# Kernel tuning notes

Hardware: AMD Instinct MI355X
Metric: run time of the kernel (lower is better)

Reference implementation:

```python
import jax, jax.numpy as jnp
import numpy as np

E, K, H, I = 32, 4, 2048, 1024   # experts, top_k, hidden, moe_intermediate
T = 4096                          # tokens (batch*seq flattened)
ROUTED_SCALING_FACTOR = 1.0


def setup_inputs() -> dict:
    key = jax.random.key(0)
    ks = jax.random.split(key, 5)
    return {
        "hidden_states": jax.random.normal(ks[0], (T, H), jnp.float32),
        "gate_w": jax.random.normal(ks[1], (E, H), jnp.float32) * 0.02,
        "expert_bias": jax.random.normal(ks[2], (E,), jnp.float32) * 0.01,
        "w13": jax.random.normal(ks[3], (E, 2 * I, H), jnp.float32) * 0.02,  # fused gate|up proj
        "w2": jax.random.normal(ks[4], (E, H, I), jnp.float32) * 0.02,       # down proj
    }


def reference(hidden_states, gate_w, expert_bias, w13, w2):
    x = hidden_states                                  # [T, H]
    router_logits = x @ gate_w.T                       # [T, E]
    scores = jax.nn.sigmoid(router_logits)             # sigmoid scoring
    # expert bias affects SELECTION only, not the combine weights
    _, topk_idx = jax.lax.top_k(scores + expert_bias[None, :], K)   # [T, K]
    topk_w = jnp.take_along_axis(scores, topk_idx, axis=1)          # [T, K] (bias-free weights)
    topk_w = topk_w / jnp.sum(topk_w, axis=1, keepdims=True)        # renormalize (norm_topk_prob)
    # dense combine matrix [T, E]: zero for unselected experts
    tok = jnp.arange(x.shape[0])[:, None]
    combine = jnp.zeros((x.shape[0], E), x.dtype).at[tok, topk_idx].set(topk_w)

    def expert_body(acc, ew):
        w13_e, w2_e, cw = ew                           # [2I,H], [H,I], [T]
        gu = x @ w13_e.T                               # [T, 2I]
        h = jax.nn.silu(gu[:, :I]) * gu[:, I:]         # SwiGLU
        return acc + cw[:, None] * (h @ w2_e.T), None  # weighted combine

    out, _ = jax.lax.scan(expert_body, jnp.zeros_like(x), (w13, w2, combine.T))
    return out * ROUTED_SCALING_FACTOR
```

## Files before the change

kernel.cpp:

```cpp
#include <hip/hip_runtime.h>

#define NE 32
#define NK 4
#define HD 2048
#define ID 1024
#define NT 4096
#define TKR (NT*NK)
#define BM 128
#define BK 64
#define LDA 72
#define MAXTILES 160

typedef __attribute__((ext_vector_type(8))) short short8;
typedef __attribute__((ext_vector_type(4))) float floatx4;

__device__ __forceinline__ unsigned short f2bf(float f) {
  unsigned u = __builtin_bit_cast(unsigned, f);
  unsigned r = u + 0x7fffu + ((u >> 16) & 1u);
  return (unsigned short)(r >> 16);
}

__global__ __launch_bounds__(256) void cvt_kernel(const float* __restrict__ x,
                                                  unsigned short* __restrict__ xb) {
  size_t i = ((size_t)blockIdx.x * 256 + threadIdx.x) * 8;
  if (i >= (size_t)NT * HD) return;
  float4 a = *(const float4*)(x + i);
  float4 b = *(const float4*)(x + i + 4);
  union { unsigned short s[8]; int4 v; } p;
  p.s[0]=f2bf(a.x); p.s[1]=f2bf(a.y); p.s[2]=f2bf(a.z); p.s[3]=f2bf(a.w);
  p.s[4]=f2bf(b.x); p.s[5]=f2bf(b.y); p.s[6]=f2bf(b.z); p.s[7]=f2bf(b.w);
  *(int4*)(xb + i) = p.v;
}

__global__ __launch_bounds__(256) void router_kernel(
    const float* __restrict__ x, const float* __restrict__ gate_w,
    const float* __restrict__ bias, int* __restrict__ topk_idx,
    float* __restrict__ topk_w, int* __restrict__ counts) {
  int t = blockIdx.x;
  int tid = threadIdx.x;
  int e = tid >> 3, l8 = tid & 7;
  const float* xr = x + (size_t)t * HD;
  const float* gr = gate_w + (size_t)e * HD;
  float s = 0.f;
  int base = l8 * 256;
#pragma unroll 8
  for (int i = 0; i < 256; i += 4) {
    float4 xv = *(const float4*)(xr + base + i);
    float4 gv = *(const float4*)(gr + base + i);
    s += xv.x*gv.x + xv.y*gv.y + xv.z*gv.z + xv.w*gv.w;
  }
  s += __shfl_down(s, 4, 64);
  s += __shfl_down(s, 2, 64);
  s += __shfl_down(s, 1, 64);
  __shared__ float sc[NE];
  if (l8 == 0) sc[e] = s;
  __syncthreads();
  if (tid == 0) {
    float sig[NE], sel[NE];
    for (int i = 0; i < NE; i++) {
      sig[i] = 1.f / (1.f + expf(-sc[i]));
      sel[i] = sig[i] + bias[i];
    }
    int idxs[NK]; float wsum = 0.f;
    for (int k = 0; k < NK; k++) {
      int bi = 0; float bv = -1e30f;
      for (int i = 0; i < NE; i++)
        if (sel[i] > bv) { bv = sel[i]; bi = i; }
      sel[bi] = -1e30f;
      idxs[k] = bi; wsum += sig[bi];
    }
    for (int k = 0; k < NK; k++) {
      topk_idx[t*NK + k] = idxs[k];
      topk_w[t*NK + k] = sig[idxs[k]] / wsum;
      atomicAdd(&counts[idxs[k]], 1);
    }
  }
}

__global__ void plan_kernel(const int* __restrict__ counts, int* __restrict__ offsets,
                            int* __restrict__ cursor, int* __restrict__ tiles,
                            int* __restrict__ numtiles) {
  if (threadIdx.x == 0) {
    int off = 0;
    for (int e = 0; e < NE; e++) { offsets[e] = off; off += counts[e]; cursor[e] = 0; }
    offsets[NE] = off;
    int nt = 0;
    for (int e = 0; e < NE; e++) {
      int start = offsets[e], n = counts[e];
      for (int r = 0; r < n; r += BM) {
        tiles[nt*3+0] = e; tiles[nt*3+1] = start + r; tiles[nt*3+2] = min(BM, n - r);
        nt++;
      }
    }
    *numtiles = nt;
  }
}

__global__ __launch_bounds__(256) void scatter_kernel(
    const int* __restrict__ topk_idx, const float* __restrict__ topk_w,
    const int* __restrict__ offsets, int* __restrict__ cursor,
    int* __restrict__ sorted_token, float* __restrict__ sorted_w) {
  int i = blockIdx.x * 256 + threadIdx.x;
  int e = topk_idx[i];
  int pos = offsets[e] + atomicAdd(&cursor[e], 1);
  sorted_token[pos] = i >> 2;
  sorted_w[pos] = topk_w[i];
}

__global__ __launch_bounds__(256) void gemm1_kernel(
    const unsigned short* __restrict__ xb, const float* __restrict__ w13,
    const int* __restrict__ tiles, const int* __restrict__ numtiles,
    const int* __restrict__ sorted_token, const float* __restrict__ sorted_w,
    unsigned short* __restrict__ hbuf) {
  int mt = blockIdx.y;
  if (mt >= *numtiles) return;
  int e = tiles[mt*3+0], g0 = tiles[mt*3+1], mrows = tiles[mt*3+2];
  int nb = blockIdx.x * 64;

  __shared__ unsigned short As[BM*LDA];
  __shared__ unsigned short Bs[BM*LDA];

  int tid = threadIdx.x;
  int wave = tid >> 6, lane = tid & 63;
  int m15 = lane & 15, q = lane >> 4;
  const float* w13e = w13 + (size_t)e * (2*ID) * HD;

  const unsigned short* aptr[4]; const float* bptr[4]; int sto[4];
#pragma unroll
  for (int i = 0; i < 4; i++) {
    int c = tid + 256*i;
    int r = c >> 3;
    int col = (c & 7) * 8;
    int rr = r < mrows ? r : 0;
    aptr[i] = xb + (size_t)sorted_token[g0+rr] * HD + col;
    int sr = (r < 64) ? (nb + r) : (ID + nb + r - 64);
    bptr[i] = w13e + (size_t)sr * HD + col;
    sto[i] = r * LDA + col;
  }

  floatx4 acc[2][8];
  floatx4 zf = {0.f,0.f,0.f,0.f};
#pragma unroll
  for (int mi=0;mi<2;mi++)
#pragma unroll
    for (int ni=0;ni<8;ni++) acc[mi][ni] = zf;

  for (int k0 = 0; k0 < HD; k0 += BK) {
    int4 av[4]; float4 b0[4], b1[4];
#pragma unroll
    for (int i = 0; i < 4; i++) {
      av[i] = *(const int4*)(aptr[i] + k0);
      b0[i] = *(const float4*)(bptr[i] + k0);
      b1[i] = *(const float4*)(bptr[i] + k0 + 4);
    }
#pragma unroll
    for (int i = 0; i < 4; i++) {
      *(int4*)(&As[sto[i]]) = av[i];
      union { unsigned short s[8]; int4 v; } p;
      p.s[0]=f2bf(b0[i].x); p.s[1]=f2bf(b0[i].y); p.s[2]=f2bf(b0[i].z); p.s[3]=f2bf(b0[i].w);
      p.s[4]=f2bf(b1[i].x); p.s[5]=f2bf(b1[i].y); p.s[6]=f2bf(b1[i].z); p.s[7]=f2bf(b1[i].w);
      *(int4*)(&Bs[sto[i]]) = p.v;
    }
    __syncthreads();
#pragma unroll
    for (int ks = 0; ks < 2; ks++) {
      int ko = ks*32 + q*8;
      short8 af[2], bfr[8];
#pragma unroll
      for (int mi = 0; mi < 2; mi++)
        af[mi] = *(const short8*)(&As[(wave*32 + 16*mi + m15)*LDA + ko]);
#pragma unroll
      for (int ni = 0; ni < 8; ni++)
        bfr[ni] = *(const short8*)(&Bs[(16*ni + m15)*LDA + ko]);
#pragma unroll
      for (int mi = 0; mi < 2; mi++)
#pragma unroll
        for (int ni = 0; ni < 8; ni++)
          acc[mi][ni] = __builtin_amdgcn_mfma_f32_16x16x32_bf16(af[mi], bfr[ni], acc[mi][ni], 0, 0, 0);
    }
    __syncthreads();
  }
#pragma unroll
  for (int mi = 0; mi < 2; mi++)
#pragma unroll
    for (int r = 0; r < 4; r++) {
      int row = wave*32 + 16*mi + q*4 + r;
      if (row < mrows) {
        int g = g0 + row;
        float wr = sorted_w[g];
        unsigned short* hr = hbuf + (size_t)g * ID + nb;
#pragma unroll
        for (int ni = 0; ni < 4; ni++) {
          float gv = acc[mi][ni][r];
          float uv = acc[mi][ni+4][r];
          float sg = gv / (1.f + __expf(-gv));
          hr[16*ni + m15] = f2bf(sg * uv * wr);
        }
      }
    }
}

__global__ __launch_bounds__(256) void gemm2_kernel(
    const unsigned short* __restrict__ hbuf, const float* __restrict__ w2,
    const int* __restrict__ tiles, const int* __restrict__ numtiles,
    const int* __restrict__ sorted_token, float* __restrict__ out) {
  int mt = blockIdx.y;
  if (mt >= *numtiles) return;
  int e = tiles[mt*3+0], g0 = tiles[mt*3+1], mrows = tiles[mt*3+2];
  int nb = blockIdx.x * BM;

  __shared__ unsigned short As[BM*LDA];
  __shared__ unsigned short Bs[BM*LDA];

  int tid = threadIdx.x;
  int wave = tid >> 6, lane = tid & 63;
  int m15 = lane & 15, q = lane >> 4;
  const float* w2e = w2 + (size_t)e * HD * ID;

  const unsigned short* aptr[4]; const float* bptr[4]; int sto[4];
#pragma unroll
  for (int i = 0; i < 4; i++) {
    int c = tid + 256*i;
    int r = c >> 3;
    int col = (c & 7) * 8;
    int rr = r < mrows ? r : 0;
    aptr[i] = hbuf + (size_t)(g0 + rr) * ID + col;
    bptr[i] = w2e + (size_t)(nb + r) * ID + col;
    sto[i] = r * LDA + col;
  }

  floatx4 acc[2][8];
  floatx4 zf = {0.f,0.f,0.f,0.f};
#pragma unroll
  for (int mi=0;mi<2;mi++)
#pragma unroll
    for (int ni=0;ni<8;ni++) acc[mi][ni] = zf;

  for (int k0 = 0; k0 < ID; k0 += BK) {
    int4 av[4]; float4 b0[4], b1[4];
#pragma unroll
    for (int i = 0; i < 4; i++) {
      av[i] = *(const int4*)(aptr[i] + k0);
      b0[i] = *(const float4*)(bptr[i] + k0);
      b1[i] = *(const float4*)(bptr[i] + k0 + 4);
    }
#pragma unroll
    for (int i = 0; i < 4; i++) {
      *(int4*)(&As[sto[i]]) = av[i];
      union { unsigned short s[8]; int4 v; } p;
      p.s[0]=f2bf(b0[i].x); p.s[1]=f2bf(b0[i].y); p.s[2]=f2bf(b0[i].z); p.s[3]=f2bf(b0[i].w);
      p.s[4]=f2bf(b1[i].x); p.s[5]=f2bf(b1[i].y); p.s[6]=f2bf(b1[i].z); p.s[7]=f2bf(b1[i].w);
      *(int4*)(&Bs[sto[i]]) = p.v;
    }
    __syncthreads();
#pragma unroll
    for (int ks = 0; ks < 2; ks++) {
      int ko = ks*32 + q*8;
      short8 af[2], bfr[8];
#pragma unroll
      for (int mi = 0; mi < 2; mi++)
        af[mi] = *(const short8*)(&As[(wave*32 + 16*mi + m15)*LDA + ko]);
#pragma unroll
      for (int ni = 0; ni < 8; ni++)
        bfr[ni] = *(const short8*)(&Bs[(16*ni + m15)*LDA + ko]);
#pragma unroll
      for (int mi = 0; mi < 2; mi++)
#pragma unroll
        for (int ni = 0; ni < 8; ni++)
          acc[mi][ni] = __builtin_amdgcn_mfma_f32_16x16x32_bf16(af[mi], bfr[ni], acc[mi][ni], 0, 0, 0);
    }
    __syncthreads();
  }
#pragma unroll
  for (int mi = 0; mi < 2; mi++)
#pragma unroll
    for (int r = 0; r < 4; r++) {
      int row = wave*32 + 16*mi + q*4 + r;
      if (row < mrows) {
        int tok = sorted_token[g0 + row];
        float* orow = out + (size_t)tok * HD + nb;
#pragma unroll
        for (int ni = 0; ni < 8; ni++)
          atomicAdd(&orow[16*ni + m15], acc[mi][ni][r]);
      }
    }
}

#define WS_COUNTS   0u
#define WS_CURSOR   128u
#define WS_OFFSETS  256u
#define WS_NUMTILES 512u
#define WS_TILES    1024u
#define WS_TOPKI    4096u
#define WS_TOPKW    (WS_TOPKI + TKR*4u)
#define WS_SORTTOK  (WS_TOPKW + TKR*4u)
#define WS_SORTW    (WS_SORTTOK + TKR*4u)
#define WS_XB       (WS_SORTW + TKR*4u)
#define WS_HBUF     (WS_XB + (size_t)NT*HD*2u)

extern "C" void kernel_launch(void* const* d_in, const int* in_sizes, int n_in,
                              void* d_out, int out_size, void* d_ws, size_t ws_size,
                              hipStream_t stream) {
  const float* x      = (const float*)d_in[0];
  const float* gate_w = (const float*)d_in[1];
  const float* bias   = (const float*)d_in[2];
  const float* w13    = (const float*)d_in[3];
  const float* w2     = (const float*)d_in[4];
  float* out = (float*)d_out;

  char* ws = (char*)d_ws;
  int*   counts   = (int*)(ws + WS_COUNTS);
  int*   cursor   = (int*)(ws + WS_CURSOR);
  int*   offsets  = (int*)(ws + WS_OFFSETS);
  int*   numtiles = (int*)(ws + WS_NUMTILES);
  int*   tiles    = (int*)(ws + WS_TILES);
  int*   topk_idx = (int*)(ws + WS_TOPKI);
  float* topk_w   = (float*)(ws + WS_TOPKW);
  int*   sorted_token = (int*)(ws + WS_SORTTOK);
  float* sorted_w     = (float*)(ws + WS_SORTW);
  unsigned short* xb   = (unsigned short*)(ws + WS_XB);
  unsigned short* hbuf = (unsigned short*)(ws + WS_HBUF);

  hipMemsetAsync(ws, 0, 1024, stream);
  hipMemsetAsync(d_out, 0, (size_t)out_size * 4, stream);

  cvt_kernel<<<NT*HD/8/256, 256, 0, stream>>>(x, xb);
  router_kernel<<<NT, 256, 0, stream>>>(x, gate_w, bias, topk_idx, topk_w, counts);
  plan_kernel<<<1, 64, 0, stream>>>(counts, offsets, cursor, tiles, numtiles);
  scatter_kernel<<<TKR/256, 256, 0, stream>>>(topk_idx, topk_w, offsets, cursor,
                                              sorted_token, sorted_w);
  gemm1_kernel<<<dim3(2*ID/BM, MAXTILES), 256, 0, stream>>>(xb, w13, tiles, numtiles,
                                                            sorted_token, sorted_w, hbuf);
  gemm2_kernel<<<dim3(HD/BM, MAXTILES), 256, 0, stream>>>(hbuf, w2, tiles, numtiles,
                                                          sorted_token, out);
}
```

Baseline: 1.542 ms.

## Pre-convert expert weights to bf16 and stage GEMM tiles via direct global-to-LDS loads

New measurement: 1.655 ms. 7.3% more time.

```diff
diff --git a/kernel.cpp b/kernel.cpp
--- a/kernel.cpp
+++ b/kernel.cpp
@@ -20,16 +20,22 @@
   return (unsigned short)(r >> 16);
 }
 
-__global__ __launch_bounds__(256) void cvt_kernel(const float* __restrict__ x,
-                                                  unsigned short* __restrict__ xb) {
-  size_t i = ((size_t)blockIdx.x * 256 + threadIdx.x) * 8;
-  if (i >= (size_t)NT * HD) return;
-  float4 a = *(const float4*)(x + i);
-  float4 b = *(const float4*)(x + i + 4);
-  union { unsigned short s[8]; int4 v; } p;
-  p.s[0]=f2bf(a.x); p.s[1]=f2bf(a.y); p.s[2]=f2bf(a.z); p.s[3]=f2bf(a.w);
-  p.s[4]=f2bf(b.x); p.s[5]=f2bf(b.y); p.s[6]=f2bf(b.z); p.s[7]=f2bf(b.w);
-  *(int4*)(xb + i) = p.v;
+#define GLOAD16(g, l) __builtin_amdgcn_global_load_lds( \
+    (const __attribute__((address_space(1))) void*)(g), \
+    (__attribute__((address_space(3))) void*)(l), 16, 0, 0)
+
+__global__ __launch_bounds__(256) void cvt_kernel(const float* __restrict__ src,
+                                                  unsigned short* __restrict__ dst,
+                                                  size_t n) {
+  size_t stride = (size_t)gridDim.x * 256 * 8;
+  for (size_t i = ((size_t)blockIdx.x * 256 + threadIdx.x) * 8; i < n; i += stride) {
+    float4 a = *(const float4*)(src + i);
+    float4 b = *(const float4*)(src + i + 4);
+    union { unsigned short s[8]; int4 v; } p;
+    p.s[0]=f2bf(a.x); p.s[1]=f2bf(a.y); p.s[2]=f2bf(a.z); p.s[3]=f2bf(a.w);
+    p.s[4]=f2bf(b.x); p.s[5]=f2bf(b.y); p.s[6]=f2bf(b.z); p.s[7]=f2bf(b.w);
+    *(int4*)(dst + i) = p.v;
+  }
 }
 
 __global__ __launch_bounds__(256) void router_kernel(
@@ -107,7 +113,177 @@
   sorted_w[pos] = topk_w[i];
 }
 
+
 __global__ __launch_bounds__(256) void gemm1_kernel(
+    const unsigned short* __restrict__ xb, const unsigned short* __restrict__ wb13,
+    const int* __restrict__ tiles, const int* __restrict__ numtiles,
+    const int* __restrict__ sorted_token, const float* __restrict__ sorted_w,
+    unsigned short* __restrict__ hbuf) {
+  int mt = blockIdx.y;
+  if (mt >= *numtiles) return;
+  int e = tiles[mt*3+0], g0 = tiles[mt*3+1], mrows = tiles[mt*3+2];
+  int nb = blockIdx.x * 64;
+
+  __shared__ unsigned short As[BM*BK];
+  __shared__ unsigned short Bs[BM*BK];
+
+  int tid = threadIdx.x;
+  int wave = tid >> 6, lane = tid & 63;
+  int m15 = lane & 15, q = lane >> 4;
+  const unsigned short* wbe = wb13 + (size_t)e * (2*ID) * HD;
+
+  const unsigned short* asrc[4]; const unsigned short* bsrc[4];
+  unsigned short* adst[4]; unsigned short* bdst[4];
+#pragma unroll
+  for (int i = 0; i < 4; i++) {
+    int c = i*256 + tid;
+    int r = c >> 3, cc = c & 7;
+    int sc = ((cc ^ (r & 7)) << 3);
+    int rr = r < mrows ? r : 0;
+    asrc[i] = xb + (size_t)sorted_token[g0+rr] * HD + sc;
+    int sr = (r < 64) ? (nb + r) : (ID + nb + r - 64);
+    bsrc[i] = wbe + (size_t)sr * HD + sc;
+    int dchunk = (i*256 + wave*64) * 8;
+    adst[i] = &As[dchunk];
+    bdst[i] = &Bs[dchunk];
+  }
+
+  floatx4 acc[2][8];
+  floatx4 zf = {0.f,0.f,0.f,0.f};
+#pragma unroll
+  for (int mi=0;mi<2;mi++)
+#pragma unroll
+    for (int ni=0;ni<8;ni++) acc[mi][ni] = zf;
+
+  for (int k0 = 0; k0 < HD; k0 += BK) {
+#pragma unroll
+    for (int i = 0; i < 4; i++) GLOAD16(asrc[i] + k0, adst[i]);
+#pragma unroll
+    for (int i = 0; i < 4; i++) GLOAD16(bsrc[i] + k0, bdst[i]);
+    __syncthreads();
+#pragma unroll
+    for (int ks = 0; ks < 2; ks++) {
+      short8 af[2], bfr[8];
+#pragma unroll
+      for (int mi = 0; mi < 2; mi++) {
+        int row = wave*32 + 16*mi + m15;
+        af[mi] = *(const short8*)(&As[row*64 + (((ks*4 + q) ^ (row & 7)) << 3)]);
+      }
+#pragma unroll
+      for (int ni = 0; ni < 8; ni++) {
+        int row = 16*ni + m15;
+        bfr[ni] = *(const short8*)(&Bs[row*64 + (((ks*4 + q) ^ (row & 7)) << 3)]);
+      }
+#pragma unroll
+      for (int mi = 0; mi < 2; mi++)
+#pragma unroll
+        for (int ni = 0; ni < 8; ni++)
+          acc[mi][ni] = __builtin_amdgcn_mfma_f32_16x16x32_bf16(af[mi], bfr[ni], acc[mi][ni], 0, 0, 0);
+    }
+    __syncthreads();
+  }
+#pragma unroll
+  for (int mi = 0; mi < 2; mi++)
+#pragma unroll
+    for (int r = 0; r < 4; r++) {
+      int row = wave*32 + 16*mi + q*4 + r;
+      if (row < mrows) {
+        int g = g0 + row;
+        float wr = sorted_w[g];
+        unsigned short* hr = hbuf + (size_t)g * ID + nb;
+#pragma unroll
+        for (int ni = 0; ni < 4; ni++) {
+          float gv = acc[mi][ni][r];
+          float uv = acc[mi][ni+4][r];
+          float sg = gv / (1.f + __expf(-gv));
+          hr[16*ni + m15] = f2bf(sg * uv * wr);
+        }
+      }
+    }
+}
+
+__global__ __launch_bounds__(256) void gemm2_kernel(
+    const unsigned short* __restrict__ hbuf, const unsigned short* __restrict__ wb2,
+    const int* __restrict__ tiles, const int* __restrict__ numtiles,
+    const int* __restrict__ sorted_token, float* __restrict__ out) {
+  int mt = blockIdx.y;
+  if (mt >= *numtiles) return;
+  int e = tiles[mt*3+0], g0 = tiles[mt*3+1], mrows = tiles[mt*3+2];
+  int nb = blockIdx.x * BM;
+
+  __shared__ unsigned short As[BM*BK];
+  __shared__ unsigned short Bs[BM*BK];
+
+  int tid = threadIdx.x;
+  int wave = tid >> 6, lane = tid & 63;
+  int m15 = lane & 15, q = lane >> 4;
+  const unsigned short* w2e = wb2 + (size_t)e * HD * ID;
+
+  const unsigned short* asrc[4]; const unsigned short* bsrc[4];
+  unsigned short* adst[4]; unsigned short* bdst[4];
+#pragma unroll
+  for (int i = 0; i < 4; i++) {
+    int c = i*256 + tid;
+    int r = c >> 3, cc = c & 7;
+    int sc = ((cc ^ (r & 7)) << 3);
+    int rr = r < mrows ? r : 0;
+    asrc[i] = hbuf + (size_t)(g0 + rr) * ID + sc;
+    bsrc[i] = w2e + (size_t)(nb + r) * ID + sc;
+    int dchunk = (i*256 + wave*64) * 8;
+    adst[i] = &As[dchunk];
+    bdst[i] = &Bs[dchunk];
+  }
+
+  floatx4 acc[2][8];
+  floatx4 zf = {0.f,0.f,0.f,0.f};
+#pragma unroll
+  for (int mi=0;mi<2;mi++)
+#pragma unroll
+    for (int ni=0;ni<8;ni++) acc[mi][ni] = zf;
+
+  for (int k0 = 0; k0 < ID; k0 += BK) {
+#pragma unroll
+    for (int i = 0; i < 4; i++) GLOAD16(asrc[i] + k0, adst[i]);
+#pragma unroll
+    for (int i = 0; i < 4; i++) GLOAD16(bsrc[i] + k0, bdst[i]);
+    __syncthreads();
+#pragma unroll
+    for (int ks = 0; ks < 2; ks++) {
+      short8 af[2], bfr[8];
+#pragma unroll
+      for (int mi = 0; mi < 2; mi++) {
+        int row = wave*32 + 16*mi + m15;
+        af[mi] = *(const short8*)(&As[row*64 + (((ks*4 + q) ^ (row & 7)) << 3)]);
+      }
+#pragma unroll
+      for (int ni = 0; ni < 8; ni++) {
+        int row = 16*ni + m15;
+        bfr[ni] = *(const short8*)(&Bs[row*64 + (((ks*4 + q) ^ (row & 7)) << 3)]);
+      }
+#pragma unroll
+      for (int mi = 0; mi < 2; mi++)
+#pragma unroll
+        for (int ni = 0; ni < 8; ni++)
+          acc[mi][ni] = __builtin_amdgcn_mfma_f32_16x16x32_bf16(af[mi], bfr[ni], acc[mi][ni], 0, 0, 0);
+    }
+    __syncthreads();
+  }
+#pragma unroll
+  for (int mi = 0; mi < 2; mi++)
+#pragma unroll
+    for (int r = 0; r < 4; r++) {
+      int row = wave*32 + 16*mi + q*4 + r;
+      if (row < mrows) {
+        int tok = sorted_token[g0 + row];
+        float* orow = out + (size_t)tok * HD + nb;
+#pragma unroll
+        for (int ni = 0; ni < 8; ni++)
+          atomicAdd(&orow[16*ni + m15], acc[mi][ni][r]);
+      }
+    }
+}
+
+__global__ __launch_bounds__(256) void gemm1_legacy(
     const unsigned short* __restrict__ xb, const float* __restrict__ w13,
     const int* __restrict__ tiles, const int* __restrict__ numtiles,
     const int* __restrict__ sorted_token, const float* __restrict__ sorted_w,
@@ -200,7 +376,7 @@
     }
 }
 
-__global__ __launch_bounds__(256) void gemm2_kernel(
+__global__ __launch_bounds__(256) void gemm2_legacy(
     const unsigned short* __restrict__ hbuf, const float* __restrict__ w2,
     const int* __restrict__ tiles, const int* __restrict__ numtiles,
     const int* __restrict__ sorted_token, float* __restrict__ out) {
@@ -297,6 +473,9 @@
 #define WS_SORTW    (WS_SORTTOK + TKR*4u)
 #define WS_XB       (WS_SORTW + TKR*4u)
 #define WS_HBUF     (WS_XB + (size_t)NT*HD*2u)
+#define WS_WB13     (WS_HBUF + (size_t)TKR*ID*2u)
+#define WS_WB2      (WS_WB13 + (size_t)NE*2*ID*HD*2u)
+#define WS_END      (WS_WB2 + (size_t)NE*HD*ID*2u)
 
 extern "C" void kernel_launch(void* const* d_in, const int* in_sizes, int n_in,
                               void* d_out, int out_size, void* d_ws, size_t ws_size,
@@ -320,17 +499,29 @@
   float* sorted_w     = (float*)(ws + WS_SORTW);
   unsigned short* xb   = (unsigned short*)(ws + WS_XB);
   unsigned short* hbuf = (unsigned short*)(ws + WS_HBUF);
+  unsigned short* wb13 = (unsigned short*)(ws + WS_WB13);
+  unsigned short* wb2  = (unsigned short*)(ws + WS_WB2);
 
   hipMemsetAsync(ws, 0, 1024, stream);
   hipMemsetAsync(d_out, 0, (size_t)out_size * 4, stream);
 
-  cvt_kernel<<<NT*HD/8/256, 256, 0, stream>>>(x, xb);
+  cvt_kernel<<<4096, 256, 0, stream>>>(x, xb, (size_t)NT*HD);
   router_kernel<<<NT, 256, 0, stream>>>(x, gate_w, bias, topk_idx, topk_w, counts);
   plan_kernel<<<1, 64, 0, stream>>>(counts, offsets, cursor, tiles, numtiles);
   scatter_kernel<<<TKR/256, 256, 0, stream>>>(topk_idx, topk_w, offsets, cursor,
                                               sorted_token, sorted_w);
-  gemm1_kernel<<<dim3(2*ID/BM, MAXTILES), 256, 0, stream>>>(xb, w13, tiles, numtiles,
-                                                            sorted_token, sorted_w, hbuf);
-  gemm2_kernel<<<dim3(HD/BM, MAXTILES), 256, 0, stream>>>(hbuf, w2, tiles, numtiles,
-                                                          sorted_token, out);
-}
+
+  if (ws_size >= WS_END) {
+    cvt_kernel<<<8192, 256, 0, stream>>>(w13, wb13, (size_t)NE*2*ID*HD);
+    cvt_kernel<<<8192, 256, 0, stream>>>(w2,  wb2,  (size_t)NE*HD*ID);
+    gemm1_kernel<<<dim3(2*ID/BM, MAXTILES), 256, 0, stream>>>(xb, wb13, tiles, numtiles,
+                                                              sorted_token, sorted_w, hbuf);
+    gemm2_kernel<<<dim3(HD/BM, MAXTILES), 256, 0, stream>>>(hbuf, wb2, tiles, numtiles,
+                                                            sorted_token, out);
+  } else {
+    gemm1_legacy<<<dim3(2*ID/BM, MAXTILES), 256, 0, stream>>>(xb, w13, tiles, numtiles,
+                                                              sorted_token, sorted_w, hbuf);
+    gemm2_legacy<<<dim3(HD/BM, MAXTILES), 256, 0, stream>>>(hbuf, w2, tiles, numtiles,
+                                                            sorted_token, out);
+  }
+}
```

## Double-buffer MoE GEMMs with direct global-to-LDS loads, swizzled LDS, XCD-aware tile order

Applied to the files above, without the earlier changes.

Measured after the change: 1.587 ms. 2.9% more time.

```diff
diff --git a/kernel.cpp b/kernel.cpp
--- a/kernel.cpp
+++ b/kernel.cpp
@@ -1,4 +1,5 @@
 #include <hip/hip_runtime.h>
+#include <hip/hip_bf16.h>
 
 #define NE 32
 #define NK 4
@@ -8,7 +9,6 @@
 #define TKR (NT*NK)
 #define BM 128
 #define BK 64
-#define LDA 72
 #define MAXTILES 160
 
 typedef __attribute__((ext_vector_type(8))) short short8;
@@ -20,16 +20,28 @@
   return (unsigned short)(r >> 16);
 }
 
-__global__ __launch_bounds__(256) void cvt_kernel(const float* __restrict__ x,
-                                                  unsigned short* __restrict__ xb) {
-  size_t i = ((size_t)blockIdx.x * 256 + threadIdx.x) * 8;
-  if (i >= (size_t)NT * HD) return;
-  float4 a = *(const float4*)(x + i);
-  float4 b = *(const float4*)(x + i + 4);
-  union { unsigned short s[8]; int4 v; } p;
-  p.s[0]=f2bf(a.x); p.s[1]=f2bf(a.y); p.s[2]=f2bf(a.z); p.s[3]=f2bf(a.w);
-  p.s[4]=f2bf(b.x); p.s[5]=f2bf(b.y); p.s[6]=f2bf(b.z); p.s[7]=f2bf(b.w);
-  *(int4*)(xb + i) = p.v;
+__device__ __forceinline__ unsigned pk2bf(float lo, float hi) {
+  unsigned short a = __builtin_bit_cast(unsigned short, __float2bfloat16(lo));
+  unsigned short b = __builtin_bit_cast(unsigned short, __float2bfloat16(hi));
+  return (unsigned)a | ((unsigned)b << 16);
+}
+
+#define GLOAD16(g, l) __builtin_amdgcn_global_load_lds( \
+    (const __attribute__((address_space(1))) void*)(g), \
+    (__attribute__((address_space(3))) void*)(l), 16, 0, 0)
+
+__global__ __launch_bounds__(256) void cvt_kernel(const float* __restrict__ src,
+                                                  unsigned short* __restrict__ dst,
+                                                  size_t n) {
+  size_t stride = (size_t)gridDim.x * 256 * 8;
+  for (size_t i = ((size_t)blockIdx.x * 256 + threadIdx.x) * 8; i < n; i += stride) {
+    float4 a = *(const float4*)(src + i);
+    float4 b = *(const float4*)(src + i + 4);
+    union { unsigned short s[8]; int4 v; } p;
+    p.s[0]=f2bf(a.x); p.s[1]=f2bf(a.y); p.s[2]=f2bf(a.z); p.s[3]=f2bf(a.w);
+    p.s[4]=f2bf(b.x); p.s[5]=f2bf(b.y); p.s[6]=f2bf(b.z); p.s[7]=f2bf(b.w);
+    *(int4*)(dst + i) = p.v;
+  }
 }
 
 __global__ __launch_bounds__(256) void router_kernel(
@@ -107,35 +119,43 @@
   sorted_w[pos] = topk_w[i];
 }
 
-__global__ __launch_bounds__(256) void gemm1_kernel(
+
+__global__ __launch_bounds__(256, 2) void gemm1_kernel(
     const unsigned short* __restrict__ xb, const float* __restrict__ w13,
     const int* __restrict__ tiles, const int* __restrict__ numtiles,
     const int* __restrict__ sorted_token, const float* __restrict__ sorted_w,
     unsigned short* __restrict__ hbuf) {
-  int mt = blockIdx.y;
+  int wg = blockIdx.x;
+  int wgs = (wg & 7) * ((16 * MAXTILES) >> 3) + (wg >> 3);
+  int mt = wgs >> 4;
+  int xcol = wgs & 15;
   if (mt >= *numtiles) return;
   int e = tiles[mt*3+0], g0 = tiles[mt*3+1], mrows = tiles[mt*3+2];
-  int nb = blockIdx.x * 64;
-
-  __shared__ unsigned short As[BM*LDA];
-  __shared__ unsigned short Bs[BM*LDA];
+  int nb = xcol * 64;
+
+  __shared__ unsigned short As0[BM*BK];
+  __shared__ unsigned short Bs0[BM*BK];
+  __shared__ unsigned short As1[BM*BK];
+  __shared__ unsigned short Bs1[BM*BK];
 
   int tid = threadIdx.x;
   int wave = tid >> 6, lane = tid & 63;
   int m15 = lane & 15, q = lane >> 4;
   const float* w13e = w13 + (size_t)e * (2*ID) * HD;
 
-  const unsigned short* aptr[4]; const float* bptr[4]; int sto[4];
+  const unsigned short* asrc[4]; const float* bsrc[4];
+  int dch[4], bsto[4];
 #pragma unroll
   for (int i = 0; i < 4; i++) {
-    int c = tid + 256*i;
-    int r = c >> 3;
-    int col = (c & 7) * 8;
+    int c = i*256 + tid;
+    int r = c >> 3, cc = c & 7;
+    int sc = ((cc ^ (r & 7)) << 3);
     int rr = r < mrows ? r : 0;
-    aptr[i] = xb + (size_t)sorted_token[g0+rr] * HD + col;
+    asrc[i] = xb + (size_t)sorted_token[g0+rr] * HD + sc;
     int sr = (r < 64) ? (nb + r) : (ID + nb + r - 64);
-    bptr[i] = w13e + (size_t)sr * HD + col;
-    sto[i] = r * LDA + col;
+    bsrc[i] = w13e + (size_t)sr * HD + cc*8;
+    dch[i]  = (i*256 + wave*64) * 8;
+    bsto[i] = r*64 + ((cc ^ (r & 7)) << 3);
   }
 
   floatx4 acc[2][8];
@@ -145,41 +165,68 @@
 #pragma unroll
     for (int ni=0;ni<8;ni++) acc[mi][ni] = zf;
 
-  for (int k0 = 0; k0 < HD; k0 += BK) {
-    int4 av[4]; float4 b0[4], b1[4];
+  float4 pb0[4], pb1[4];
+  auto stageA = [&](unsigned short* dst, int k) {
+#pragma unroll
+    for (int i = 0; i < 4; i++) GLOAD16(asrc[i] + k, dst + dch[i]);
+  };
+  auto loadB = [&](int k) {
 #pragma unroll
     for (int i = 0; i < 4; i++) {
-      av[i] = *(const int4*)(aptr[i] + k0);
-      b0[i] = *(const float4*)(bptr[i] + k0);
-      b1[i] = *(const float4*)(bptr[i] + k0 + 4);
-    }
+      pb0[i] = *(const float4*)(bsrc[i] + k);
+      pb1[i] = *(const float4*)(bsrc[i] + k + 4);
+    }
+  };
+  auto writeB = [&](unsigned short* Bsb) {
 #pragma unroll
     for (int i = 0; i < 4; i++) {
-      *(int4*)(&As[sto[i]]) = av[i];
-      union { unsigned short s[8]; int4 v; } p;
-      p.s[0]=f2bf(b0[i].x); p.s[1]=f2bf(b0[i].y); p.s[2]=f2bf(b0[i].z); p.s[3]=f2bf(b0[i].w);
-      p.s[4]=f2bf(b1[i].x); p.s[5]=f2bf(b1[i].y); p.s[6]=f2bf(b1[i].z); p.s[7]=f2bf(b1[i].w);
-      *(int4*)(&Bs[sto[i]]) = p.v;
-    }
-    __syncthreads();
+      union { unsigned u[4]; int4 v; } p;
+      p.u[0] = pk2bf(pb0[i].x, pb0[i].y);
+      p.u[1] = pk2bf(pb0[i].z, pb0[i].w);
+      p.u[2] = pk2bf(pb1[i].x, pb1[i].y);
+      p.u[3] = pk2bf(pb1[i].z, pb1[i].w);
+      *(int4*)(Bsb + bsto[i]) = p.v;
+    }
+  };
+  auto compute = [&](const unsigned short* Asb, const unsigned short* Bsb) {
 #pragma unroll
     for (int ks = 0; ks < 2; ks++) {
-      int ko = ks*32 + q*8;
       short8 af[2], bfr[8];
 #pragma unroll
-      for (int mi = 0; mi < 2; mi++)
-        af[mi] = *(const short8*)(&As[(wave*32 + 16*mi + m15)*LDA + ko]);
-#pragma unroll
-      for (int ni = 0; ni < 8; ni++)
-        bfr[ni] = *(const short8*)(&Bs[(16*ni + m15)*LDA + ko]);
+      for (int mi = 0; mi < 2; mi++) {
+        int row = wave*32 + 16*mi + m15;
+        af[mi] = *(const short8*)(Asb + row*64 + (((ks*4 + q) ^ (row & 7)) << 3));
+      }
+#pragma unroll
+      for (int ni = 0; ni < 8; ni++) {
+        int row = 16*ni + m15;
+        bfr[ni] = *(const short8*)(Bsb + row*64 + (((ks*4 + q) ^ (row & 7)) << 3));
+      }
 #pragma unroll
       for (int mi = 0; mi < 2; mi++)
 #pragma unroll
         for (int ni = 0; ni < 8; ni++)
           acc[mi][ni] = __builtin_amdgcn_mfma_f32_16x16x32_bf16(af[mi], bfr[ni], acc[mi][ni], 0, 0, 0);
     }
+  };
+
+  stageA(As0, 0);
+  loadB(0); writeB(Bs0);
+  __syncthreads();
+  constexpr int NS2 = HD / (2*BK);
+  for (int t = 0; t < NS2; ++t) {
+    int kA = t * 2 * BK;
+    stageA(As1, kA + BK); loadB(kA + BK);
+    compute(As0, Bs0);
+    writeB(Bs1);
     __syncthreads();
-  }
+    bool more = (t + 1 < NS2);
+    if (more) { stageA(As0, kA + 2*BK); loadB(kA + 2*BK); }
+    compute(As1, Bs1);
+    if (more) writeB(Bs0);
+    __syncthreads();
+  }
+
 #pragma unroll
   for (int mi = 0; mi < 2; mi++)
 #pragma unroll
@@ -200,33 +247,40 @@
     }
 }
 
-__global__ __launch_bounds__(256) void gemm2_kernel(
+__global__ __launch_bounds__(256, 2) void gemm2_kernel(
     const unsigned short* __restrict__ hbuf, const float* __restrict__ w2,
     const int* __restrict__ tiles, const int* __restrict__ numtiles,
     const int* __restrict__ sorted_token, float* __restrict__ out) {
-  int mt = blockIdx.y;
+  int wg = blockIdx.x;
+  int wgs = (wg & 7) * ((16 * MAXTILES) >> 3) + (wg >> 3);
+  int mt = wgs >> 4;
+  int xcol = wgs & 15;
   if (mt >= *numtiles) return;
   int e = tiles[mt*3+0], g0 = tiles[mt*3+1], mrows = tiles[mt*3+2];
-  int nb = blockIdx.x * BM;
-
-  __shared__ unsigned short As[BM*LDA];
-  __shared__ unsigned short Bs[BM*LDA];
+  int nb = xcol * BM;
+
+  __shared__ unsigned short As0[BM*BK];
+  __shared__ unsigned short Bs0[BM*BK];
+  __shared__ unsigned short As1[BM*BK];
+  __shared__ unsigned short Bs1[BM*BK];
 
   int tid = threadIdx.x;
   int wave = tid >> 6, lane = tid & 63;
   int m15 = lane & 15, q = lane >> 4;
   const float* w2e = w2 + (size_t)e * HD * ID;
 
-  const unsigned short* aptr[4]; const float* bptr[4]; int sto[4];
+  const unsigned short* asrc[4]; const float* bsrc[4];
+  int dch[4], bsto[4];
 #pragma unroll
   for (int i = 0; i < 4; i++) {
-    int c = tid + 256*i;
-    int r = c >> 3;
-    int col = (c & 7) * 8;
+    int c = i*256 + tid;
+    int r = c >> 3, cc = c & 7;
+    int sc = ((cc ^ (r & 7)) << 3);
     int rr = r < mrows ? r : 0;
-    aptr[i] = hbuf + (size_t)(g0 + rr) * ID + col;
-    bptr[i] = w2e + (size_t)(nb + r) * ID + col;
-    sto[i] = r * LDA + col;
+    asrc[i] = hbuf + (size_t)(g0 + rr) * ID + sc;
+    bsrc[i] = w2e + (size_t)(nb + r) * ID + cc*8;
+    dch[i]  = (i*256 + wave*64) * 8;
+    bsto[i] = r*64 + ((cc ^ (r & 7)) << 3);
   }
 
   floatx4 acc[2][8];
@@ -236,41 +290,68 @@
 #pragma unroll
     for (int ni=0;ni<8;ni++) acc[mi][ni] = zf;
 
-  for (int k0 = 0; k0 < ID; k0 += BK) {
-    int4 av[4]; float4 b0[4], b1[4];
+  float4 pb0[4], pb1[4];
+  auto stageA = [&](unsigned short* dst, int k) {
+#pragma unroll
+    for (int i = 0; i < 4; i++) GLOAD16(asrc[i] + k, dst + dch[i]);
+  };
+  auto loadB = [&](int k) {
 #pragma unroll
     for (int i = 0; i < 4; i++) {
-      av[i] = *(const int4*)(aptr[i] + k0);
-      b0[i] = *(const float4*)(bptr[i] + k0);
-      b1[i] = *(const float4*)(bptr[i] + k0 + 4);
-    }
+      pb0[i] = *(const float4*)(bsrc[i] + k);
+      pb1[i] = *(const float4*)(bsrc[i] + k + 4);
+    }
+  };
+  auto writeB = [&](unsigned short* Bsb) {
 #pragma unroll
     for (int i = 0; i < 4; i++) {
-      *(int4*)(&As[sto[i]]) = av[i];
-      union { unsigned short s[8]; int4 v; } p;
-      p.s[0]=f2bf(b0[i].x); p.s[1]=f2bf(b0[i].y); p.s[2]=f2bf(b0[i].z); p.s[3]=f2bf(b0[i].w);
-      p.s[4]=f2bf(b1[i].x); p.s[5]=f2bf(b1[i].y); p.s[6]=f2bf(b1[i].z); p.s[7]=f2bf(b1[i].w);
-      *(int4*)(&Bs[sto[i]]) = p.v;
-    }
-    __syncthreads();
+      union { unsigned u[4]; int4 v; } p;
+      p.u[0] = pk2bf(pb0[i].x, pb0[i].y);
+      p.u[1] = pk2bf(pb0[i].z, pb0[i].w);
+      p.u[2] = pk2bf(pb1[i].x, pb1[i].y);
+      p.u[3] = pk2bf(pb1[i].z, pb1[i].w);
+      *(int4*)(Bsb + bsto[i]) = p.v;
+    }
+  };
+  auto compute = [&](const unsigned short* Asb, const unsigned short* Bsb) {
 #pragma unroll
     for (int ks = 0; ks < 2; ks++) {
-      int ko = ks*32 + q*8;
       short8 af[2], bfr[8];
 #pragma unroll
-      for (int mi = 0; mi < 2; mi++)
-        af[mi] = *(const short8*)(&As[(wave*32 + 16*mi + m15)*LDA + ko]);
-#pragma unroll
-      for (int ni = 0; ni < 8; ni++)
-        bfr[ni] = *(const short8*)(&Bs[(16*ni + m15)*LDA + ko]);
+      for (int mi = 0; mi < 2; mi++) {
+        int row = wave*32 + 16*mi + m15;
+        af[mi] = *(const short8*)(Asb + row*64 + (((ks*4 + q) ^ (row & 7)) << 3));
+      }
+#pragma unroll
+      for (int ni = 0; ni < 8; ni++) {
+        int row = 16*ni + m15;
+        bfr[ni] = *(const short8*)(Bsb + row*64 + (((ks*4 + q) ^ (row & 7)) << 3));
+      }
 #pragma unroll
       for (int mi = 0; mi < 2; mi++)
 #pragma unroll
         for (int ni = 0; ni < 8; ni++)
           acc[mi][ni] = __builtin_amdgcn_mfma_f32_16x16x32_bf16(af[mi], bfr[ni], acc[mi][ni], 0, 0, 0);
     }
+  };
+
+  stageA(As0, 0);
+  loadB(0); writeB(Bs0);
+  __syncthreads();
+  constexpr int NS2 = ID / (2*BK);
+  for (int t = 0; t < NS2; ++t) {
+    int kA = t * 2 * BK;
+    stageA(As1, kA + BK); loadB(kA + BK);
+    compute(As0, Bs0);
+    writeB(Bs1);
     __syncthreads();
-  }
+    bool more = (t + 1 < NS2);
+    if (more) { stageA(As0, kA + 2*BK); loadB(kA + 2*BK); }
+    compute(As1, Bs1);
+    if (more) writeB(Bs0);
+    __syncthreads();
+  }
+
 #pragma unroll
   for (int mi = 0; mi < 2; mi++)
 #pragma unroll
@@ -324,13 +405,13 @@
   hipMemsetAsync(ws, 0, 1024, stream);
   hipMemsetAsync(d_out, 0, (size_t)out_size * 4, stream);
 
-  cvt_kernel<<<NT*HD/8/256, 256, 0, stream>>>(x, xb);
+  cvt_kernel<<<4096, 256, 0, stream>>>(x, xb, (size_t)NT*HD);
   router_kernel<<<NT, 256, 0, stream>>>(x, gate_w, bias, topk_idx, topk_w, counts);
   plan_kernel<<<1, 64, 0, stream>>>(counts, offsets, cursor, tiles, numtiles);
   scatter_kernel<<<TKR/256, 256, 0, stream>>>(topk_idx, topk_w, offsets, cursor,
                                               sorted_token, sorted_w);
-  gemm1_kernel<<<dim3(2*ID/BM, MAXTILES), 256, 0, stream>>>(xb, w13, tiles, numtiles,
-                                                            sorted_token, sorted_w, hbuf);
-  gemm2_kernel<<<dim3(HD/BM, MAXTILES), 256, 0, stream>>>(hbuf, w2, tiles, numtiles,
-                                                          sorted_token, out);
-}
+  gemm1_kernel<<<16*MAXTILES, 256, 0, stream>>>(xb, w13, tiles, numtiles,
+                                                sorted_token, sorted_w, hbuf);
+  gemm2_kernel<<<16*MAXTILES, 256, 0, stream>>>(hbuf, w2, tiles, numtiles,
+                                                sorted_token, out);
+}
```
